# Kernel tuning notes

Measured on AMD Instinct MI355X. Metric: run time of the kernel, lower is better.

The kernel has to match this reference:

```python
import jax, jax.numpy as jnp
import numpy as np

T = 3          # hparams['T'] message-passing iterations
E = 100000     # num edges (rows of link_state)
M = 200000     # num message pairs
D = 128        # hidden dim of link_state / GRU units
H = 256        # Message MLP hidden width
G = 64         # num graphs


def setup_inputs() -> dict:
    key = jax.random.key(0)
    ks = jax.random.split(key, 16)
    s = 0.05
    inp = {
        'link_state': jax.random.normal(ks[0], (E, D), jnp.float32),
        'states_first': jax.random.randint(ks[1], (M,), 0, E),
        'states_second': jax.random.randint(ks[2], (M,), 0, E),
        'states_graph_ids': jnp.sort(jax.random.randint(ks[3], (E,), 0, G)),
        'sates_num_edges': E,
        # Message MLP: Dense(H, relu) -> Dense(D, relu)
        'mW1': jax.random.normal(ks[4], (2 * D, H), jnp.float32) * s,
        'mb1': jnp.zeros((H,), jnp.float32),
        'mW2': jax.random.normal(ks[5], (H, D), jnp.float32) * s,
        'mb2': jnp.zeros((D,), jnp.float32),
        # GRUCell (keras, reset_after=True): kernel [D,3D], recurrent [D,3D], bias [2,3D]
        'gru_kernel': jax.random.normal(ks[6], (D, 3 * D), jnp.float32) * s,
        'gru_recurrent': jax.random.normal(ks[7], (D, 3 * D), jnp.float32) * s,
        'gru_bias': jnp.zeros((2, 3 * D), jnp.float32),
        # Readout MLP: Dense(H, relu) -> Dense(H, relu) -> Dense(1)
        'rW1': jax.random.normal(ks[8], (D, H), jnp.float32) * s,
        'rb1': jnp.zeros((H,), jnp.float32),
        'rW2': jax.random.normal(ks[9], (H, H), jnp.float32) * s,
        'rb2': jnp.zeros((H,), jnp.float32),
        'rW3': jax.random.normal(ks[10], (H, 1), jnp.float32) * s,
        'rb3': jnp.zeros((1,), jnp.float32),
    }
    return inp


def _gru_step(x, h, kernel, recurrent, bias):
    # keras GRUCell with reset_after=True; gate order: z, r, h
    mx = x @ kernel + bias[0]          # [N, 3D]
    mh = h @ recurrent + bias[1]       # [N, 3D]
    xz, xr, xh = jnp.split(mx, 3, axis=-1)
    hz, hr, hh = jnp.split(mh, 3, axis=-1)
    z = jax.nn.sigmoid(xz + hz)
    r = jax.nn.sigmoid(xr + hr)
    hcand = jnp.tanh(xh + r * hh)
    return z * h + (1.0 - z) * hcand


def reference(link_state, states_first, states_second, states_graph_ids,
              sates_num_edges, mW1, mb1, mW2, mb2,
              gru_kernel, gru_recurrent, gru_bias,
              rW1, rb1, rW2, rb2, rW3, rb3):
    for _ in range(T):
        main_e = link_state[states_first]        # [M, D] gather
        neigh_e = link_state[states_second]      # [M, D] gather
        concat = jnp.concatenate([main_e, neigh_e], axis=1)  # [M, 2D]
        msg = jax.nn.relu(concat @ mW1 + mb1)
        msg = jax.nn.relu(msg @ mW2 + mb2)       # [M, D]
        edges_inputs = jax.ops.segment_sum(msg, states_second,
                                           num_segments=sates_num_edges)  # [E, D]
        link_state = _gru_step(edges_inputs, link_state,
                               gru_kernel, gru_recurrent, gru_bias)
    graph_state = jax.ops.segment_sum(link_state, states_graph_ids,
                                      num_segments=G)  # [G, D]
    r = jax.nn.relu(graph_state @ rW1 + rb1)
    r = jax.nn.relu(r @ rW2 + rb2)
    return r @ rW3 + rb3  # [G, 1]
```

## Files before the change

### kernel.cpp

```cpp
#include <hip/hip_runtime.h>

#define NUM_E 100000
#define NUM_M 200000
#define DIM   128
#define HID   256
#define NG    64
#define TITER 3
#define NB_SCAN 98
#define GS_ER 128
#define TM    64

typedef __attribute__((ext_vector_type(8))) short bf16x8;
typedef __attribute__((ext_vector_type(4))) float f32x4;

__device__ __forceinline__ unsigned short f2bf(float f) {
  unsigned u = __float_as_uint(f);
  u += 0x7FFF + ((u >> 16) & 1);
  return (unsigned short)(u >> 16);
}
__device__ __forceinline__ float bf2f(unsigned short h) {
  return __uint_as_float(((unsigned)h) << 16);
}
__device__ __forceinline__ float sigmoidf_(float v) {
  return 1.f / (1.f + __expf(-v));
}
__device__ __forceinline__ float tanhf_(float u) {
  u = fminf(fmaxf(u, -15.f), 15.f);
  float ex = __expf(-2.f * u);
  return (1.f - ex) / (1.f + ex);
}
__device__ __forceinline__ float relu_(float v) { return fmaxf(v, 0.f); }

__device__ __forceinline__ void acc8(float* xs, bf16x8 v) {
  #pragma unroll
  for (int j = 0; j < 8; ++j) xs[j] += bf2f((unsigned short)v[j]);
}

__device__ __forceinline__ int swzm(int row, int col) {
  return row * 256 + (col ^ ((row & 7) << 3));
}
__device__ __forceinline__ int swzg(int row, int col) {
  return row * 128 + (col ^ ((row & 7) << 3));
}

#define MFMA(a, b, c) __builtin_amdgcn_mfma_f32_16x16x32_bf16((a), (b), (c), 0, 0, 0)

__global__ __launch_bounds__(256) void scan1_kernel(const int* __restrict__ counts,
                                                    int* __restrict__ partials) {
  __shared__ int sh[256];
  int b = blockIdx.x, t = threadIdx.x;
  int i0 = b * 1024 + t * 4;
  int c0 = (i0 + 0 < NUM_E) ? counts[i0 + 0] : 0;
  int c1 = (i0 + 1 < NUM_E) ? counts[i0 + 1] : 0;
  int c2 = (i0 + 2 < NUM_E) ? counts[i0 + 2] : 0;
  int c3 = (i0 + 3 < NUM_E) ? counts[i0 + 3] : 0;
  int tsum = c0 + c1 + c2 + c3;
  sh[t] = tsum;
  __syncthreads();
  for (int off = 1; off < 256; off <<= 1) {
    int v = (t >= off) ? sh[t - off] : 0;
    __syncthreads();
    sh[t] += v;
    __syncthreads();
  }
  if (t == 255) partials[b] = sh[255];
}

__global__ void scan2_kernel(const int* __restrict__ partials, int* __restrict__ base,
                             int* __restrict__ rowptr) {
  if (threadIdx.x == 0) {
    int run = 0;
    for (int b = 0; b < NB_SCAN; ++b) { base[b] = run; run += partials[b]; }
    rowptr[NUM_E] = NUM_M;
  }
}

__global__ __launch_bounds__(256) void scan3_kernel(const int* __restrict__ counts,
                                                    const int* __restrict__ base,
                                                    int* __restrict__ rowptr) {
  __shared__ int sh[256];
  int b = blockIdx.x, t = threadIdx.x;
  int i0 = b * 1024 + t * 4;
  int c0 = (i0 + 0 < NUM_E) ? counts[i0 + 0] : 0;
  int c1 = (i0 + 1 < NUM_E) ? counts[i0 + 1] : 0;
  int c2 = (i0 + 2 < NUM_E) ? counts[i0 + 2] : 0;
  int c3 = (i0 + 3 < NUM_E) ? counts[i0 + 3] : 0;
  int tsum = c0 + c1 + c2 + c3;
  sh[t] = tsum;
  __syncthreads();
  for (int off = 1; off < 256; off <<= 1) {
    int v = (t >= off) ? sh[t - off] : 0;
    __syncthreads();
    sh[t] += v;
    __syncthreads();
  }
  int p = base[b] + (sh[t] - tsum);
  if (i0 + 0 < NUM_E) rowptr[i0 + 0] = p;
  if (i0 + 1 < NUM_E) rowptr[i0 + 1] = p + c0;
  if (i0 + 2 < NUM_E) rowptr[i0 + 2] = p + c0 + c1;
  if (i0 + 3 < NUM_E) rowptr[i0 + 3] = p + c0 + c1 + c2;
}

__global__ void scatter_kernel(const int* __restrict__ second,
                               const int* __restrict__ rowptr,
                               int* __restrict__ cursor, int* __restrict__ order) {
  int m = blockIdx.x * blockDim.x + threadIdx.x;
  if (m < NUM_M) {
    int e = second[m];
    int pos = atomicAdd(&cursor[e], 1);
    int idx = rowptr[e] + pos;
    if (idx < rowptr[e + 1]) order[idx] = m;
  }
}

__device__ __forceinline__ void pack_range(
    const float* __restrict__ srcA, const float* __restrict__ srcB, int KrowsA,
    int N, int src_ld, int col_off, unsigned short* __restrict__ dst, int idx) {
  int l = idx & 63;
  int t = idx >> 6;
  int NF = N / 16;
  int nf = t % NF;
  int ks = t / NF;
  int n = nf * 16 + (l & 15) + col_off;
  int k0 = ks * 32 + (l >> 4) * 8;
  unsigned short o[8];
  #pragma unroll
  for (int j = 0; j < 8; ++j) {
    int k = k0 + j;
    const float* src = (k < KrowsA) ? (srcA + (size_t)k * src_ld)
                                    : (srcB + (size_t)(k - KrowsA) * src_ld);
    o[j] = f2bf(src[n]);
  }
  ushort4* d = (ushort4*)(dst + (size_t)idx * 8);
  d[0] = make_ushort4(o[0], o[1], o[2], o[3]);
  d[1] = make_ushort4(o[4], o[5], o[6], o[7]);
}

__global__ __launch_bounds__(256) void prep_kernel(
    const float4* __restrict__ ls4, ushort4* __restrict__ lsb4, int n4,
    const int* __restrict__ second, int* __restrict__ counts,
    float4* __restrict__ gs4,
    const float* __restrict__ mW1, const float* __restrict__ mW2,
    const float* __restrict__ gk,  const float* __restrict__ gr,
    unsigned short* __restrict__ W1p,  unsigned short* __restrict__ W2p,
    unsigned short* __restrict__ Wzrp, unsigned short* __restrict__ Wkhp,
    unsigned short* __restrict__ Wrhp) {
  int i = blockIdx.x * 256 + threadIdx.x;
  if (i < n4) {
    float4 v = ls4[i];
    ushort4 o;
    o.x = f2bf(v.x); o.y = f2bf(v.y); o.z = f2bf(v.z); o.w = f2bf(v.w);
    lsb4[i] = o;
  }
  if (i < NUM_M) atomicAdd(&counts[second[i]], 1);
  if (i < NG * DIM / 4) gs4[i] = make_float4(0.f, 0.f, 0.f, 0.f);
  if      (i < 8192)  pack_range(mW1, mW1, 256, 256, 256, 0,   W1p,  i);
  else if (i < 12288) pack_range(mW2, mW2, 256, 128, 128, 0,   W2p,  i - 8192);
  else if (i < 20480) pack_range(gk,  gr,  128, 256, 384, 0,   Wzrp, i - 12288);
  else if (i < 22528) pack_range(gk,  gk,  128, 128, 384, 256, Wkhp, i - 20480);
  else if (i < 24576) pack_range(gr,  gr,  128, 128, 384, 256, Wrhp, i - 22528);
}

__global__ __launch_bounds__(512, 2) void msg_kernel(
    const unsigned short* __restrict__ lsb,
    const int* __restrict__ first, const int* __restrict__ second,
    const int* __restrict__ order,
    const unsigned short* __restrict__ W1p,
    const float* __restrict__ b1,
    const unsigned short* __restrict__ W2p,
    const float* __restrict__ b2,
    unsigned short* __restrict__ msgout)
{
  __shared__ unsigned short actL[2][TM * 256];
  __shared__ unsigned short h1s[2][TM * 256];

  const int tid  = threadIdx.x;
  const int wave = tid >> 6;
  const int lane = tid & 63;
  const int c    = lane & 15;
  const int quad = lane >> 4;

  const int sr  = tid >> 5;
  const int shf = (tid >> 4) & 1;
  const int si  = tid & 15;

  const bf16x8* W1f = (const bf16x8*)W1p;
  const bf16x8* W2f = (const bf16x8*)W2p;
  bf16x8 w1r[16];
  #pragma unroll
  for (int ks = 0; ks < 8; ++ks)
    #pragma unroll
    for (int i = 0; i < 2; ++i)
      w1r[ks * 2 + i] = W1f[(ks * 16 + wave * 2 + i) * 64 + lane];
  bf16x8 w2r[8];
  #pragma unroll
  for (int ks = 0; ks < 8; ++ks)
    w2r[ks] = W2f[(ks * 8 + wave) * 64 + lane];

  float4 b1v[2];
  #pragma unroll
  for (int i = 0; i < 2; ++i)
    b1v[i] = *(const float4*)(b1 + (wave * 2 + i) * 16 + quad * 4);
  float4 b2v = *(const float4*)(b2 + wave * 16 + quad * 4);

  const int nTiles = NUM_M / TM;
  const int stride = gridDim.x;
  int tile = blockIdx.x;
  if (tile >= nTiles) return;
  int parity = 0;

  {
    #pragma unroll
    for (int k = 0; k < 4; ++k) {
      int m = order[tile * TM + sr + k * 16];
      int e = shf ? second[m] : first[m];
      bf16x8 v = *(const bf16x8*)(lsb + (size_t)e * DIM + si * 8);
      *(bf16x8*)&actL[0][swzm(sr + k * 16, shf * 128 + si * 8)] = v;
    }
  }
  int en[4] = {0, 0, 0, 0};
  {
    int t1 = tile + stride;
    if (t1 < nTiles) {
      #pragma unroll
      for (int k = 0; k < 4; ++k) {
        int m = order[t1 * TM + sr + k * 16];
        en[k] = shf ? second[m] : first[m];
      }
    }
  }
  __syncthreads();

  while (true) {
    const int m0 = tile * TM;
    const int next  = tile + stride;
    const int next2 = next + stride;
    const bool have_next  = (next < nTiles);
    const bool have_next2 = (next2 < nTiles);

    bf16x8 sv[4];
    if (have_next) {
      #pragma unroll
      for (int k = 0; k < 4; ++k)
        sv[k] = *(const bf16x8*)(lsb + (size_t)en[k] * DIM + si * 8);
    }
    int o[4] = {0, 0, 0, 0};
    if (have_next2) {
      #pragma unroll
      for (int k = 0; k < 4; ++k)
        o[k] = order[next2 * TM + sr + k * 16];
    }

    const unsigned short* ab = &actL[parity][0];
    f32x4 acc[4][2];
    #pragma unroll
    for (int s = 0; s < 4; ++s) { acc[s][0] = (f32x4)(0.f); acc[s][1] = (f32x4)(0.f); }
    #pragma unroll
    for (int ks = 0; ks < 8; ++ks) {
      #pragma unroll
      for (int s = 0; s < 4; ++s) {
        bf16x8 b = *(const bf16x8*)&ab[swzm(s * 16 + c, ks * 32 + quad * 8)];
        acc[s][0] = MFMA(w1r[ks * 2 + 0], b, acc[s][0]);
        acc[s][1] = MFMA(w1r[ks * 2 + 1], b, acc[s][1]);
      }
    }

    if (have_next2) {
      #pragma unroll
      for (int k = 0; k < 4; ++k)
        en[k] = shf ? second[o[k]] : first[o[k]];
    }

    if (have_next) {
      unsigned short* aw = &actL[parity ^ 1][0];
      #pragma unroll
      for (int k = 0; k < 4; ++k)
        *(bf16x8*)&aw[swzm(sr + k * 16, shf * 128 + si * 8)] = sv[k];
    }

    unsigned short* hb = &h1s[parity][0];
    #pragma unroll
    for (int i = 0; i < 2; ++i) {
      int n0 = (wave * 2 + i) * 16 + quad * 4;
      #pragma unroll
      for (int s = 0; s < 4; ++s) {
        ushort4 pk;
        pk.x = f2bf(relu_(acc[s][i][0] + b1v[i].x));
        pk.y = f2bf(relu_(acc[s][i][1] + b1v[i].y));
        pk.z = f2bf(relu_(acc[s][i][2] + b1v[i].z));
        pk.w = f2bf(relu_(acc[s][i][3] + b1v[i].w));
        *(ushort4*)&hb[swzm(s * 16 + c, n0)] = pk;
      }
    }
    __syncthreads();

    f32x4 a2[4];
    #pragma unroll
    for (int s = 0; s < 4; ++s) a2[s] = (f32x4)(0.f);
    #pragma unroll
    for (int ks2 = 0; ks2 < 8; ++ks2) {
      #pragma unroll
      for (int s = 0; s < 4; ++s) {
        bf16x8 b = *(const bf16x8*)&hb[swzm(s * 16 + c, ks2 * 32 + quad * 8)];
        a2[s] = MFMA(w2r[ks2], b, a2[s]);
      }
    }

    {
      int n0 = wave * 16 + quad * 4;
      #pragma unroll
      for (int s = 0; s < 4; ++s) {
        ushort4 pk;
        pk.x = f2bf(relu_(a2[s][0] + b2v.x));
        pk.y = f2bf(relu_(a2[s][1] + b2v.y));
        pk.z = f2bf(relu_(a2[s][2] + b2v.z));
        pk.w = f2bf(relu_(a2[s][3] + b2v.w));
        *(ushort4*)(msgout + (size_t)(m0 + s * 16 + c) * DIM + n0) = pk;
      }
    }

    if (!have_next) break;
    tile = next;
    parity ^= 1;
  }
}

__device__ __forceinline__ ushort4 gru_gate(
    f32x4 az, f32x4 ar, f32x4 axh, f32x4 ahh, ushort4 hraw,
    float4 bz0, float4 br0, float4 bh0, float4 bz1, float4 br1, float4 bh1) {
  float ho[4] = { bf2f(hraw.x), bf2f(hraw.y), bf2f(hraw.z), bf2f(hraw.w) };
  const float* paz  = (const float*)&az;  const float* par  = (const float*)&ar;
  const float* paxh = (const float*)&axh; const float* pahh = (const float*)&ahh;
  const float* pz0 = (const float*)&bz0; const float* pr0 = (const float*)&br0;
  const float* ph0 = (const float*)&bh0; const float* pz1 = (const float*)&bz1;
  const float* pr1 = (const float*)&br1; const float* ph1 = (const float*)&bh1;
  unsigned short o[4];
  #pragma unroll
  for (int j = 0; j < 4; ++j) {
    float z  = sigmoidf_(paz[j] + pz0[j] + pz1[j]);
    float r  = sigmoidf_(par[j] + pr0[j] + pr1[j]);
    float hc = tanhf_(paxh[j] + ph0[j] + r * (pahh[j] + ph1[j]));
    o[j] = f2bf(z * ho[j] + (1.f - z) * hc);
  }
  return make_ushort4(o[0], o[1], o[2], o[3]);
}

__global__ __launch_bounds__(512, 2) void gru_kernel(
    const unsigned short* __restrict__ msgb,
    const int* __restrict__ rowptr,
    unsigned short* __restrict__ lsb,
    const unsigned short* __restrict__ Wzrp,
    const unsigned short* __restrict__ Wkhp,
    const unsigned short* __restrict__ Wrhp,
    const float* __restrict__ gb)
{
  __shared__ unsigned short xfL[2][32 * 128];
  __shared__ unsigned short hfL[2][32 * 128];

  const int tid  = threadIdx.x;
  const int wave = tid >> 6;
  const int lane = tid & 63;
  const int c    = lane & 15;
  const int quad = lane >> 4;

  const bf16x8* Wzrf = (const bf16x8*)Wzrp;
  const bf16x8* Wkhf = (const bf16x8*)Wkhp;
  const bf16x8* Wrhf = (const bf16x8*)Wrhp;
  bf16x8 wz[8], wr[8];
  #pragma unroll
  for (int ks = 0; ks < 8; ++ks) {
    wz[ks] = Wzrf[(ks * 16 + wave) * 64 + lane];
    wr[ks] = Wzrf[(ks * 16 + 8 + wave) * 64 + lane];
  }
  bf16x8 wxh[4], whh[4];
  #pragma unroll
  for (int ks = 0; ks < 4; ++ks) {
    wxh[ks] = Wkhf[(ks * 8 + wave) * 64 + lane];
    whh[ks] = Wrhf[(ks * 8 + wave) * 64 + lane];
  }

  const float4* gbv = (const float4*)gb;
  const int q4 = wave * 4 + quad;
  const float4 b0z = gbv[q4],      b0r = gbv[32 + q4],  b0h = gbv[64 + q4];
  const float4 b1z = gbv[96 + q4], b1r = gbv[128 + q4], b1h = gbv[160 + q4];

  const int el = wave * 4 + (lane >> 4);
  const int li = lane & 15;

  const int nTiles = NUM_E / 32;
  const int stride = gridDim.x;
  int tile = blockIdx.x;
  if (tile >= nTiles) return;
  int par = 0;

  {
    const int e  = tile * 32 + el;
    const int rs = rowptr[e], re = rowptr[e + 1];
    float xs[8];
    #pragma unroll
    for (int j = 0; j < 8; ++j) xs[j] = 0.f;
    bf16x8 hrow = *(const bf16x8*)(lsb + (size_t)e * DIM + li * 8);
    for (int p0 = rs; p0 < re; p0 += 8) {
      const int pm = re - 1;
      bf16x8 tv[8];
      #pragma unroll
      for (int k = 0; k < 8; ++k)
        tv[k] = *(const bf16x8*)(msgb + (size_t)min(p0 + k, pm) * DIM + li * 8);
      #pragma unroll
      for (int k = 0; k < 8; ++k)
        if (p0 + k < re) acc8(xs, tv[k]);
    }
    bf16x8 xv;
    #pragma unroll
    for (int j = 0; j < 8; ++j) xv[j] = (short)f2bf(xs[j]);
    *(bf16x8*)&xfL[0][swzg(el, li * 8)] = xv;
    *(bf16x8*)&hfL[0][swzg(el, li * 8)] = hrow;
  }
  int rs1 = 0, re1 = 0;
  if (tile + stride < nTiles) {
    const int e1 = (tile + stride) * 32 + el;
    rs1 = rowptr[e1]; re1 = rowptr[e1 + 1];
  }
  __syncthreads();

  while (true) {
    const int nextT = tile + stride;
    const bool have_next  = (nextT < nTiles);
    const bool have_next2 = (nextT + stride < nTiles);

    bf16x8 r0, r1, r2, r3, r4, r5, r6, r7, hrow;
    if (have_next) {
      const int e1 = nextT * 32 + el;
      const int pc = min(max(re1 - 1, rs1), NUM_M - 1);
      r0 = *(const bf16x8*)(msgb + (size_t)min(rs1 + 0, pc) * DIM + li * 8);
      r1 = *(const bf16x8*)(msgb + (size_t)min(rs1 + 1, pc) * DIM + li * 8);
      r2 = *(const bf16x8*)(msgb + (size_t)min(rs1 + 2, pc) * DIM + li * 8);
      r3 = *(const bf16x8*)(msgb + (size_t)min(rs1 + 3, pc) * DIM + li * 8);
      r4 = *(const bf16x8*)(msgb + (size_t)min(rs1 + 4, pc) * DIM + li * 8);
      r5 = *(const bf16x8*)(msgb + (size_t)min(rs1 + 5, pc) * DIM + li * 8);
      r6 = *(const bf16x8*)(msgb + (size_t)min(rs1 + 6, pc) * DIM + li * 8);
      r7 = *(const bf16x8*)(msgb + (size_t)min(rs1 + 7, pc) * DIM + li * 8);
      hrow = *(const bf16x8*)(lsb + (size_t)e1 * DIM + li * 8);
    }
    int rs2 = 0, re2 = 0;
    if (have_next2) {
      const int e2 = (nextT + stride) * 32 + el;
      rs2 = rowptr[e2]; re2 = rowptr[e2 + 1];
    }

    const unsigned short* xb = &xfL[par][0];
    const unsigned short* hb = &hfL[par][0];
    f32x4 zA = (f32x4)(0.f), zB = (f32x4)(0.f);
    f32x4 rA = (f32x4)(0.f), rB = (f32x4)(0.f);
    f32x4 xhA = (f32x4)(0.f), xhB = (f32x4)(0.f);
    f32x4 hhA = (f32x4)(0.f), hhB = (f32x4)(0.f);
    #pragma unroll
    for (int ks = 0; ks < 4; ++ks) {
      bf16x8 xA = *(const bf16x8*)&xb[swzg(c,      ks * 32 + quad * 8)];
      bf16x8 xB = *(const bf16x8*)&xb[swzg(16 + c, ks * 32 + quad * 8)];
      bf16x8 hA = *(const bf16x8*)&hb[swzg(c,      ks * 32 + quad * 8)];
      bf16x8 hB = *(const bf16x8*)&hb[swzg(16 + c, ks * 32 + quad * 8)];
      zA  = MFMA(wz[ks],     xA, zA);   zB  = MFMA(wz[ks],     xB, zB);
      rA  = MFMA(wr[ks],     xA, rA);   rB  = MFMA(wr[ks],     xB, rB);
      zA  = MFMA(wz[4 + ks], hA, zA);   zB  = MFMA(wz[4 + ks], hB, zB);
      rA  = MFMA(wr[4 + ks], hA, rA);   rB  = MFMA(wr[4 + ks], hB, rB);
      xhA = MFMA(wxh[ks],    xA, xhA);  xhB = MFMA(wxh[ks],    xB, xhB);
      hhA = MFMA(whh[ks],    hA, hhA);  hhB = MFMA(whh[ks],    hB, hhB);
    }
    {
      const int n0 = wave * 16 + quad * 4;
      ushort4 hrawA = *(const ushort4*)&hb[swzg(c,      n0)];
      ushort4 hrawB = *(const ushort4*)&hb[swzg(16 + c, n0)];
      ushort4 pkA = gru_gate(zA, rA, xhA, hhA, hrawA, b0z, b0r, b0h, b1z, b1r, b1h);
      ushort4 pkB = gru_gate(zB, rB, xhB, hhB, hrawB, b0z, b0r, b0h, b1z, b1r, b1h);
      *(ushort4*)(lsb + (size_t)(tile * 32 + c) * DIM + n0)      = pkA;
      *(ushort4*)(lsb + (size_t)(tile * 32 + 16 + c) * DIM + n0) = pkB;
    }

    if (have_next) {
      float xs[8];
      #pragma unroll
      for (int j = 0; j < 8; ++j) xs[j] = 0.f;
      if (rs1 + 0 < re1) acc8(xs, r0);
      if (rs1 + 1 < re1) acc8(xs, r1);
      if (rs1 + 2 < re1) acc8(xs, r2);
      if (rs1 + 3 < re1) acc8(xs, r3);
      if (rs1 + 4 < re1) acc8(xs, r4);
      if (rs1 + 5 < re1) acc8(xs, r5);
      if (rs1 + 6 < re1) acc8(xs, r6);
      if (rs1 + 7 < re1) acc8(xs, r7);
      for (int p0 = rs1 + 8; p0 < re1; p0 += 8) {
        const int pm = re1 - 1;
        bf16x8 tv[8];
        #pragma unroll
        for (int k = 0; k < 8; ++k)
          tv[k] = *(const bf16x8*)(msgb + (size_t)min(p0 + k, pm) * DIM + li * 8);
        #pragma unroll
        for (int k = 0; k < 8; ++k)
          if (p0 + k < re1) acc8(xs, tv[k]);
      }
      bf16x8 xv;
      #pragma unroll
      for (int j = 0; j < 8; ++j) xv[j] = (short)f2bf(xs[j]);
      *(bf16x8*)&xfL[par ^ 1][swzg(el, li * 8)] = xv;
      *(bf16x8*)&hfL[par ^ 1][swzg(el, li * 8)] = hrow;
    }
    __syncthreads();
    if (!have_next) break;
    tile = nextT;
    par ^= 1;
    rs1 = rs2;
    re1 = re2;
  }
}

__global__ __launch_bounds__(256) void graph_sum_kernel(
    const unsigned short* __restrict__ lsb, const int* __restrict__ gids,
    float* __restrict__ gs) {
  const int t = threadIdx.x;
  const int d = t & 127;
  const int half = t >> 7;
  const int e0 = blockIdx.x * GS_ER;
  const int e1 = min(e0 + GS_ER, NUM_E);
  float acc = 0.f;
  int cur = -1;
  for (int e = e0 + half; e < e1; e += 2) {
    int g = gids[e];
    if (g != cur) {
      if (cur >= 0) atomicAdd(&gs[cur * DIM + d], acc);
      acc = 0.f;
      cur = g;
    }
    acc += bf2f(lsb[(size_t)e * DIM + d]);
  }
  if (cur >= 0) atomicAdd(&gs[cur * DIM + d], acc);
}

__global__ __launch_bounds__(256) void readout_kernel(
    const float* __restrict__ gs,
    const float* __restrict__ rW1, const float* __restrict__ rb1,
    const float* __restrict__ rW2, const float* __restrict__ rb2,
    const float* __restrict__ rW3, const float* __restrict__ rb3,
    float* __restrict__ out) {
  __shared__ float shg[DIM];
  __shared__ float sh1[HID];
  __shared__ float red[HID];
  int g = blockIdx.x, c = threadIdx.x;
  if (c < DIM) shg[c] = gs[g * DIM + c];
  __syncthreads();
  float s = rb1[c];
  for (int k = 0; k < DIM; ++k) s += shg[k] * rW1[k * HID + c];
  sh1[c] = relu_(s);
  __syncthreads();
  s = rb2[c];
  for (int k = 0; k < HID; ++k) s += sh1[k] * rW2[k * HID + c];
  red[c] = relu_(s) * rW3[c];
  __syncthreads();
  for (int off = 128; off > 0; off >>= 1) {
    if (c < off) red[c] += red[c + off];
    __syncthreads();
  }
  if (c == 0) out[g] = red[0] + rb3[0];
}

extern "C" void kernel_launch(void* const* d_in, const int* in_sizes, int n_in,
                              void* d_out, int out_size, void* d_ws, size_t ws_size,
                              hipStream_t stream) {
  float* ls          = (float*)d_in[0];
  const int* first   = (const int*)d_in[1];
  const int* second  = (const int*)d_in[2];
  const int* gids    = (const int*)d_in[3];
  const float* mW1   = (const float*)d_in[5];
  const float* mb1   = (const float*)d_in[6];
  const float* mW2   = (const float*)d_in[7];
  const float* mb2   = (const float*)d_in[8];
  const float* gk    = (const float*)d_in[9];
  const float* gr    = (const float*)d_in[10];
  const float* gb    = (const float*)d_in[11];
  const float* rW1   = (const float*)d_in[12];
  const float* rb1   = (const float*)d_in[13];
  const float* rW2   = (const float*)d_in[14];
  const float* rb2   = (const float*)d_in[15];
  const float* rW3   = (const float*)d_in[16];
  const float* rb3   = (const float*)d_in[17];
  float* out = (float*)d_out;

  char* w = (char*)d_ws;
  unsigned short* msgb = (unsigned short*)w;    w += (size_t)NUM_M * DIM * 2;
  unsigned short* lsb  = (unsigned short*)w;    w += (size_t)NUM_E * DIM * 2;
  float* gs    = (float*)w;                     w += NG * DIM * 4;
  int* counts  = (int*)w;                       w += NUM_E * 4;
  int* cursor  = (int*)w;                       w += NUM_E * 4;
  int* rowptr  = (int*)w;                       w += (NUM_E + 4) * 4;
  int* order   = (int*)w;                       w += NUM_M * 4;
  int* partials= (int*)w;                       w += NB_SCAN * 4;
  int* basep   = (int*)w;                       w += NB_SCAN * 4;
  unsigned short* W1p  = (unsigned short*)w;    w += 256 * 256 * 2;
  unsigned short* W2p  = (unsigned short*)w;    w += 256 * 128 * 2;
  unsigned short* Wzrp = (unsigned short*)w;    w += 256 * 256 * 2;
  unsigned short* Wkhp = (unsigned short*)w;    w += 128 * 128 * 2;
  unsigned short* Wrhp = (unsigned short*)w;    w += 128 * 128 * 2;

  hipMemsetAsync(counts, 0, 2 * (size_t)NUM_E * 4, stream);
  const int n4 = NUM_E * DIM / 4;
  prep_kernel<<<(n4 + 255) / 256, 256, 0, stream>>>(
      (const float4*)ls, (ushort4*)lsb, n4, second, counts, (float4*)gs,
      mW1, mW2, gk, gr, W1p, W2p, Wzrp, Wkhp, Wrhp);

  scan1_kernel<<<NB_SCAN, 256, 0, stream>>>(counts, partials);
  scan2_kernel<<<1, 64, 0, stream>>>(partials, basep, rowptr);
  scan3_kernel<<<NB_SCAN, 256, 0, stream>>>(counts, basep, rowptr);
  scatter_kernel<<<(NUM_M + 255) / 256, 256, 0, stream>>>(second, rowptr, cursor, order);

  for (int t = 0; t < TITER; ++t) {
    msg_kernel<<<256, 512, 0, stream>>>(lsb, first, second, order, W1p, mb1, W2p, mb2, msgb);
    gru_kernel<<<256, 512, 0, stream>>>(msgb, rowptr, lsb, Wzrp, Wkhp, Wrhp, gb);
  }
  graph_sum_kernel<<<(NUM_E + GS_ER - 1) / GS_ER, 256, 0, stream>>>(lsb, gids, gs);
  readout_kernel<<<NG, HID, 0, stream>>>(gs, rW1, rb1, rW2, rb2, rW3, rb3, out);
}
```

Before: 492.7 us.

## Fuse message/GRU iterations and readout into one persistent kernel with grid barriers

Replaces the six per-iteration msg/GRU launches plus the graph-sum and readout launches with one persistent 256-block kernel that separates phases using an atomic-counter grid barrier. Shared memory is reused between phases, and register weight loads are kept inside each phase through an opaque zero offset. This removes launch gaps and tail effects between kernels. In exchange it depends on all 256 blocks being co-resident for the spin barrier, and it loses the restrict qualifiers.

After: 1.029 ms. +108.9%, slower.

```diff
diff --git a/kernel.cpp b/kernel.cpp
--- a/kernel.cpp
+++ b/kernel.cpp
@@ -44,6 +44,17 @@
 }
 
 #define MFMA(a, b, c) __builtin_amdgcn_mfma_f32_16x16x32_bf16((a), (b), (c), 0, 0, 0)
+
+__device__ __forceinline__ void gsync(int* bar, int target) {
+  __threadfence();
+  __syncthreads();
+  if (threadIdx.x == 0) {
+    atomicAdd(bar, 1);
+    while (__hip_atomic_load(bar, __ATOMIC_ACQUIRE, __HIP_MEMORY_SCOPE_AGENT) < target)
+      __builtin_amdgcn_s_sleep(8);
+  }
+  __syncthreads();
+}
 
 __global__ __launch_bounds__(256) void scan1_kernel(const int* __restrict__ counts,
                                                     int* __restrict__ partials) {
@@ -139,13 +150,14 @@
 __global__ __launch_bounds__(256) void prep_kernel(
     const float4* __restrict__ ls4, ushort4* __restrict__ lsb4, int n4,
     const int* __restrict__ second, int* __restrict__ counts,
-    float4* __restrict__ gs4,
+    float4* __restrict__ gs4, int* __restrict__ bar,
     const float* __restrict__ mW1, const float* __restrict__ mW2,
     const float* __restrict__ gk,  const float* __restrict__ gr,
     unsigned short* __restrict__ W1p,  unsigned short* __restrict__ W2p,
     unsigned short* __restrict__ Wzrp, unsigned short* __restrict__ Wkhp,
     unsigned short* __restrict__ Wrhp) {
   int i = blockIdx.x * 256 + threadIdx.x;
+  if (i == 0) *bar = 0;
   if (i < n4) {
     float4 v = ls4[i];
     ushort4 o;
@@ -161,25 +173,19 @@
   else if (i < 24576) pack_range(gr,  gr,  128, 128, 384, 256, Wrhp, i - 22528);
 }
 
-__global__ __launch_bounds__(512, 2) void msg_kernel(
-    const unsigned short* __restrict__ lsb,
-    const int* __restrict__ first, const int* __restrict__ second,
-    const int* __restrict__ order,
-    const unsigned short* __restrict__ W1p,
-    const float* __restrict__ b1,
-    const unsigned short* __restrict__ W2p,
-    const float* __restrict__ b2,
-    unsigned short* __restrict__ msgout)
+__device__ __forceinline__ void msg_phase(
+    unsigned short* act0, unsigned short* act1,
+    unsigned short* h10,  unsigned short* h11,
+    const unsigned short* lsb, const int* first, const int* second,
+    const int* order, const unsigned short* W1p, const float* b1,
+    const unsigned short* W2p, const float* b2, unsigned short* msgout,
+    int zero)
 {
-  __shared__ unsigned short actL[2][TM * 256];
-  __shared__ unsigned short h1s[2][TM * 256];
-
   const int tid  = threadIdx.x;
   const int wave = tid >> 6;
   const int lane = tid & 63;
   const int c    = lane & 15;
   const int quad = lane >> 4;
-
   const int sr  = tid >> 5;
   const int shf = (tid >> 4) & 1;
   const int si  = tid & 15;
@@ -191,17 +197,17 @@
   for (int ks = 0; ks < 8; ++ks)
     #pragma unroll
     for (int i = 0; i < 2; ++i)
-      w1r[ks * 2 + i] = W1f[(ks * 16 + wave * 2 + i) * 64 + lane];
+      w1r[ks * 2 + i] = W1f[(ks * 16 + wave * 2 + i) * 64 + lane + zero];
   bf16x8 w2r[8];
   #pragma unroll
   for (int ks = 0; ks < 8; ++ks)
-    w2r[ks] = W2f[(ks * 8 + wave) * 64 + lane];
+    w2r[ks] = W2f[(ks * 8 + wave) * 64 + lane + zero];
 
   float4 b1v[2];
   #pragma unroll
   for (int i = 0; i < 2; ++i)
-    b1v[i] = *(const float4*)(b1 + (wave * 2 + i) * 16 + quad * 4);
-  float4 b2v = *(const float4*)(b2 + wave * 16 + quad * 4);
+    b1v[i] = *(const float4*)(b1 + (wave * 2 + i) * 16 + quad * 4 + zero);
+  float4 b2v = *(const float4*)(b2 + wave * 16 + quad * 4 + zero);
 
   const int nTiles = NUM_M / TM;
   const int stride = gridDim.x;
@@ -215,7 +221,7 @@
       int m = order[tile * TM + sr + k * 16];
       int e = shf ? second[m] : first[m];
       bf16x8 v = *(const bf16x8*)(lsb + (size_t)e * DIM + si * 8);
-      *(bf16x8*)&actL[0][swzm(sr + k * 16, shf * 128 + si * 8)] = v;
+      *(bf16x8*)&act0[swzm(sr + k * 16, shf * 128 + si * 8)] = v;
     }
   }
   int en[4] = {0, 0, 0, 0};
@@ -251,7 +257,7 @@
         o[k] = order[next2 * TM + sr + k * 16];
     }
 
-    const unsigned short* ab = &actL[parity][0];
+    const unsigned short* ab = parity ? act1 : act0;
     f32x4 acc[4][2];
     #pragma unroll
     for (int s = 0; s < 4; ++s) { acc[s][0] = (f32x4)(0.f); acc[s][1] = (f32x4)(0.f); }
@@ -272,13 +278,13 @@
     }
 
     if (have_next) {
-      unsigned short* aw = &actL[parity ^ 1][0];
+      unsigned short* aw = parity ? act0 : act1;
       #pragma unroll
       for (int k = 0; k < 4; ++k)
         *(bf16x8*)&aw[swzm(sr + k * 16, shf * 128 + si * 8)] = sv[k];
     }
 
-    unsigned short* hb = &h1s[parity][0];
+    unsigned short* hb = parity ? h11 : h10;
     #pragma unroll
     for (int i = 0; i < 2; ++i) {
       int n0 = (wave * 2 + i) * 16 + quad * 4;
@@ -345,18 +351,13 @@
   return make_ushort4(o[0], o[1], o[2], o[3]);
 }
 
-__global__ __launch_bounds__(512, 2) void gru_kernel(
-    const unsigned short* __restrict__ msgb,
-    const int* __restrict__ rowptr,
-    unsigned short* __restrict__ lsb,
-    const unsigned short* __restrict__ Wzrp,
-    const unsigned short* __restrict__ Wkhp,
-    const unsigned short* __restrict__ Wrhp,
-    const float* __restrict__ gb)
+__device__ __forceinline__ void gru_phase(
+    unsigned short* xf0, unsigned short* xf1,
+    unsigned short* hf0, unsigned short* hf1,
+    const unsigned short* msgb, const int* rowptr, unsigned short* lsb,
+    const unsigned short* Wzrp, const unsigned short* Wkhp,
+    const unsigned short* Wrhp, const float* gb, int zero)
 {
-  __shared__ unsigned short xfL[2][32 * 128];
-  __shared__ unsigned short hfL[2][32 * 128];
-
   const int tid  = threadIdx.x;
   const int wave = tid >> 6;
   const int lane = tid & 63;
@@ -369,18 +370,18 @@
   bf16x8 wz[8], wr[8];
   #pragma unroll
   for (int ks = 0; ks < 8; ++ks) {
-    wz[ks] = Wzrf[(ks * 16 + wave) * 64 + lane];
-    wr[ks] = Wzrf[(ks * 16 + 8 + wave) * 64 + lane];
+    wz[ks] = Wzrf[(ks * 16 + wave) * 64 + lane + zero];
+    wr[ks] = Wzrf[(ks * 16 + 8 + wave) * 64 + lane + zero];
   }
   bf16x8 wxh[4], whh[4];
   #pragma unroll
   for (int ks = 0; ks < 4; ++ks) {
-    wxh[ks] = Wkhf[(ks * 8 + wave) * 64 + lane];
-    whh[ks] = Wrhf[(ks * 8 + wave) * 64 + lane];
+    wxh[ks] = Wkhf[(ks * 8 + wave) * 64 + lane + zero];
+    whh[ks] = Wrhf[(ks * 8 + wave) * 64 + lane + zero];
   }
 
   const float4* gbv = (const float4*)gb;
-  const int q4 = wave * 4 + quad;
+  const int q4 = wave * 4 + quad + zero;
   const float4 b0z = gbv[q4],      b0r = gbv[32 + q4],  b0h = gbv[64 + q4];
   const float4 b1z = gbv[96 + q4], b1r = gbv[128 + q4], b1h = gbv[160 + q4];
 
@@ -413,8 +414,8 @@
     bf16x8 xv;
     #pragma unroll
     for (int j = 0; j < 8; ++j) xv[j] = (short)f2bf(xs[j]);
-    *(bf16x8*)&xfL[0][swzg(el, li * 8)] = xv;
-    *(bf16x8*)&hfL[0][swzg(el, li * 8)] = hrow;
+    *(bf16x8*)&xf0[swzg(el, li * 8)] = xv;
+    *(bf16x8*)&hf0[swzg(el, li * 8)] = hrow;
   }
   int rs1 = 0, re1 = 0;
   if (tile + stride < nTiles) {
@@ -448,8 +449,8 @@
       rs2 = rowptr[e2]; re2 = rowptr[e2 + 1];
     }
 
-    const unsigned short* xb = &xfL[par][0];
-    const unsigned short* hb = &hfL[par][0];
+    const unsigned short* xb = par ? xf1 : xf0;
+    const unsigned short* hb = par ? hf1 : hf0;
     f32x4 zA = (f32x4)(0.f), zB = (f32x4)(0.f);
     f32x4 rA = (f32x4)(0.f), rB = (f32x4)(0.f);
     f32x4 xhA = (f32x4)(0.f), xhB = (f32x4)(0.f);
@@ -502,8 +503,10 @@
       bf16x8 xv;
       #pragma unroll
       for (int j = 0; j < 8; ++j) xv[j] = (short)f2bf(xs[j]);
-      *(bf16x8*)&xfL[par ^ 1][swzg(el, li * 8)] = xv;
-      *(bf16x8*)&hfL[par ^ 1][swzg(el, li * 8)] = hrow;
+      unsigned short* xw = par ? xf0 : xf1;
+      unsigned short* hw = par ? hf0 : hf1;
+      *(bf16x8*)&xw[swzg(el, li * 8)] = xv;
+      *(bf16x8*)&hw[swzg(el, li * 8)] = hrow;
     }
     __syncthreads();
     if (!have_next) break;
@@ -514,53 +517,80 @@
   }
 }
 
-__global__ __launch_bounds__(256) void graph_sum_kernel(
-    const unsigned short* __restrict__ lsb, const int* __restrict__ gids,
-    float* __restrict__ gs) {
-  const int t = threadIdx.x;
-  const int d = t & 127;
-  const int half = t >> 7;
-  const int e0 = blockIdx.x * GS_ER;
-  const int e1 = min(e0 + GS_ER, NUM_E);
-  float acc = 0.f;
-  int cur = -1;
-  for (int e = e0 + half; e < e1; e += 2) {
-    int g = gids[e];
-    if (g != cur) {
+__global__ __launch_bounds__(512, 2) void loop_kernel(
+    unsigned short* lsb, const int* first, const int* second, const int* order,
+    const unsigned short* W1p, const float* mb1,
+    const unsigned short* W2p, const float* mb2,
+    unsigned short* msgb, const int* rowptr,
+    const unsigned short* Wzrp, const unsigned short* Wkhp,
+    const unsigned short* Wrhp, const float* gb,
+    const int* gids, float* gs,
+    const float* rW1, const float* rb1, const float* rW2, const float* rb2,
+    const float* rW3, const float* rb3, float* out, int* bar)
+{
+  __shared__ unsigned short smA[2][TM * 256];
+  __shared__ unsigned short smB[2][TM * 256];
+
+  int phase = 0;
+  for (int it = 0; it < TITER; ++it) {
+    int z1 = 0; asm volatile("" : "+v"(z1));
+    msg_phase(&smA[0][0], &smA[1][0], &smB[0][0], &smB[1][0],
+              lsb, first, second, order, W1p, mb1, W2p, mb2, msgb, z1);
+    ++phase; gsync(bar, 256 * phase);
+    int z2 = 0; asm volatile("" : "+v"(z2));
+    gru_phase(&smA[0][0], &smA[0][4096], &smA[1][0], &smA[1][4096],
+              msgb, rowptr, lsb, Wzrp, Wkhp, Wrhp, gb, z2);
+    ++phase; gsync(bar, 256 * phase);
+  }
+
+  {
+    const int t = threadIdx.x;
+    const int d = t & 127;
+    const int q = t >> 7;
+    for (int ch = blockIdx.x; ch < (NUM_E + GS_ER - 1) / GS_ER; ch += gridDim.x) {
+      const int e0 = ch * GS_ER;
+      const int e1 = min(e0 + GS_ER, NUM_E);
+      float acc = 0.f;
+      int cur = -1;
+      for (int e = e0 + q; e < e1; e += 4) {
+        int g = gids[e];
+        if (g != cur) {
+          if (cur >= 0) atomicAdd(&gs[cur * DIM + d], acc);
+          acc = 0.f;
+          cur = g;
+        }
+        acc += bf2f(lsb[(size_t)e * DIM + d]);
+      }
       if (cur >= 0) atomicAdd(&gs[cur * DIM + d], acc);
-      acc = 0.f;
-      cur = g;
-    }
-    acc += bf2f(lsb[(size_t)e * DIM + d]);
-  }
-  if (cur >= 0) atomicAdd(&gs[cur * DIM + d], acc);
-}
-
-__global__ __launch_bounds__(256) void readout_kernel(
-    const float* __restrict__ gs,
-    const float* __restrict__ rW1, const float* __restrict__ rb1,
-    const float* __restrict__ rW2, const float* __restrict__ rb2,
-    const float* __restrict__ rW3, const float* __restrict__ rb3,
-    float* __restrict__ out) {
-  __shared__ float shg[DIM];
-  __shared__ float sh1[HID];
-  __shared__ float red[HID];
-  int g = blockIdx.x, c = threadIdx.x;
-  if (c < DIM) shg[c] = gs[g * DIM + c];
-  __syncthreads();
-  float s = rb1[c];
-  for (int k = 0; k < DIM; ++k) s += shg[k] * rW1[k * HID + c];
-  sh1[c] = relu_(s);
-  __syncthreads();
-  s = rb2[c];
-  for (int k = 0; k < HID; ++k) s += sh1[k] * rW2[k * HID + c];
-  red[c] = relu_(s) * rW3[c];
-  __syncthreads();
-  for (int off = 128; off > 0; off >>= 1) {
-    if (c < off) red[c] += red[c + off];
-    __syncthreads();
-  }
-  if (c == 0) out[g] = red[0] + rb3[0];
+    }
+  }
+  ++phase; gsync(bar, 256 * phase);
+
+  if (blockIdx.x < NG) {
+    float* shg = (float*)&smA[0][0];
+    float* sh1 = shg + DIM;
+    float* red = sh1 + HID;
+    const int g = blockIdx.x, c = threadIdx.x;
+    if (c < DIM) shg[c] = gs[g * DIM + c];
+    __syncthreads();
+    if (c < HID) {
+      float s = rb1[c];
+      for (int k = 0; k < DIM; ++k) s += shg[k] * rW1[k * HID + c];
+      sh1[c] = relu_(s);
+    }
+    __syncthreads();
+    if (c < HID) {
+      float s = rb2[c];
+      for (int k = 0; k < HID; ++k) s += sh1[k] * rW2[k * HID + c];
+      red[c] = relu_(s) * rW3[c];
+    }
+    __syncthreads();
+    for (int off = 128; off > 0; off >>= 1) {
+      if (c < off) red[c] += red[c + off];
+      __syncthreads();
+    }
+    if (c == 0) out[g] = red[0] + rb3[0];
+  }
 }
 
 extern "C" void kernel_launch(void* const* d_in, const int* in_sizes, int n_in,
@@ -595,6 +625,7 @@
   int* order   = (int*)w;                       w += NUM_M * 4;
   int* partials= (int*)w;                       w += NB_SCAN * 4;
   int* basep   = (int*)w;                       w += NB_SCAN * 4;
+  int* bar     = (int*)w;                       w += 16;
   unsigned short* W1p  = (unsigned short*)w;    w += 256 * 256 * 2;
   unsigned short* W2p  = (unsigned short*)w;    w += 256 * 128 * 2;
   unsigned short* Wzrp = (unsigned short*)w;    w += 256 * 256 * 2;
@@ -604,7 +635,7 @@
   hipMemsetAsync(counts, 0, 2 * (size_t)NUM_E * 4, stream);
   const int n4 = NUM_E * DIM / 4;
   prep_kernel<<<(n4 + 255) / 256, 256, 0, stream>>>(
-      (const float4*)ls, (ushort4*)lsb, n4, second, counts, (float4*)gs,
+      (const float4*)ls, (ushort4*)lsb, n4, second, counts, (float4*)gs, bar,
       mW1, mW2, gk, gr, W1p, W2p, Wzrp, Wkhp, Wrhp);
 
   scan1_kernel<<<NB_SCAN, 256, 0, stream>>>(counts, partials);
@@ -612,10 +643,7 @@
   scan3_kernel<<<NB_SCAN, 256, 0, stream>>>(counts, basep, rowptr);
   scatter_kernel<<<(NUM_M + 255) / 256, 256, 0, stream>>>(second, rowptr, cursor, order);
 
-  for (int t = 0; t < TITER; ++t) {
-    msg_kernel<<<256, 512, 0, stream>>>(lsb, first, second, order, W1p, mb1, W2p, mb2, msgb);
-    gru_kernel<<<256, 512, 0, stream>>>(msgb, rowptr, lsb, Wzrp, Wkhp, Wrhp, gb);
-  }
-  graph_sum_kernel<<<(NUM_E + GS_ER - 1) / GS_ER, 256, 0, stream>>>(lsb, gids, gs);
-  readout_kernel<<<NG, HID, 0, stream>>>(gs, rW1, rb1, rW2, rb2, rW3, rb3, out);
-}
+  loop_kernel<<<256, 512, 0, stream>>>(
+      lsb, first, second, order, W1p, mb1, W2p, mb2, msgb, rowptr,
+      Wzrp, Wkhp, Wrhp, gb, gids, gs, rW1, rb1, rW2, rb2, rW3, rb3, out, bar);
+}
```

## Store first/second pairs in CSR order and fuse graph sum into readout

Applied to the files above, without the earlier changes.

The scatter step now writes (first, second) index pairs in sorted order, so the message kernel reads one int2 instead of chasing order→first/second. The graph-level segment sum is folded into the readout kernel: each block binary-searches its graph's range in the sorted ids and reduces rows locally. This removes a launch, the zeroing of the accumulator and the global atomics. The trade-off is that the reduction now runs on only 64 blocks, which limits memory parallelism.

Result: slower. 590.3 us (+19.8%).

```diff
diff --git a/kernel.cpp b/kernel.cpp
--- a/kernel.cpp
+++ b/kernel.cpp
@@ -7,7 +7,6 @@
 #define NG    64
 #define TITER 3
 #define NB_SCAN 98
-#define GS_ER 128
 #define TM    64
 
 typedef __attribute__((ext_vector_type(8))) short bf16x8;
@@ -101,15 +100,16 @@
   if (i0 + 3 < NUM_E) rowptr[i0 + 3] = p + c0 + c1 + c2;
 }
 
-__global__ void scatter_kernel(const int* __restrict__ second,
+__global__ void scatter_kernel(const int* __restrict__ first,
+                               const int* __restrict__ second,
                                const int* __restrict__ rowptr,
-                               int* __restrict__ cursor, int* __restrict__ order) {
+                               int* __restrict__ cursor, int2* __restrict__ fs) {
   int m = blockIdx.x * blockDim.x + threadIdx.x;
   if (m < NUM_M) {
     int e = second[m];
     int pos = atomicAdd(&cursor[e], 1);
     int idx = rowptr[e] + pos;
-    if (idx < rowptr[e + 1]) order[idx] = m;
+    if (idx < rowptr[e + 1]) fs[idx] = make_int2(first[m], e);
   }
 }
 
@@ -139,7 +139,6 @@
 __global__ __launch_bounds__(256) void prep_kernel(
     const float4* __restrict__ ls4, ushort4* __restrict__ lsb4, int n4,
     const int* __restrict__ second, int* __restrict__ counts,
-    float4* __restrict__ gs4,
     const float* __restrict__ mW1, const float* __restrict__ mW2,
     const float* __restrict__ gk,  const float* __restrict__ gr,
     unsigned short* __restrict__ W1p,  unsigned short* __restrict__ W2p,
@@ -153,7 +152,6 @@
     lsb4[i] = o;
   }
   if (i < NUM_M) atomicAdd(&counts[second[i]], 1);
-  if (i < NG * DIM / 4) gs4[i] = make_float4(0.f, 0.f, 0.f, 0.f);
   if      (i < 8192)  pack_range(mW1, mW1, 256, 256, 256, 0,   W1p,  i);
   else if (i < 12288) pack_range(mW2, mW2, 256, 128, 128, 0,   W2p,  i - 8192);
   else if (i < 20480) pack_range(gk,  gr,  128, 256, 384, 0,   Wzrp, i - 12288);
@@ -163,8 +161,7 @@
 
 __global__ __launch_bounds__(512, 2) void msg_kernel(
     const unsigned short* __restrict__ lsb,
-    const int* __restrict__ first, const int* __restrict__ second,
-    const int* __restrict__ order,
+    const int2* __restrict__ fs,
     const unsigned short* __restrict__ W1p,
     const float* __restrict__ b1,
     const unsigned short* __restrict__ W2p,
@@ -212,8 +209,8 @@
   {
     #pragma unroll
     for (int k = 0; k < 4; ++k) {
-      int m = order[tile * TM + sr + k * 16];
-      int e = shf ? second[m] : first[m];
+      int2 p = fs[tile * TM + sr + k * 16];
+      int e = shf ? p.y : p.x;
       bf16x8 v = *(const bf16x8*)(lsb + (size_t)e * DIM + si * 8);
       *(bf16x8*)&actL[0][swzm(sr + k * 16, shf * 128 + si * 8)] = v;
     }
@@ -224,8 +221,8 @@
     if (t1 < nTiles) {
       #pragma unroll
       for (int k = 0; k < 4; ++k) {
-        int m = order[t1 * TM + sr + k * 16];
-        en[k] = shf ? second[m] : first[m];
+        int2 p = fs[t1 * TM + sr + k * 16];
+        en[k] = shf ? p.y : p.x;
       }
     }
   }
@@ -244,11 +241,11 @@
       for (int k = 0; k < 4; ++k)
         sv[k] = *(const bf16x8*)(lsb + (size_t)en[k] * DIM + si * 8);
     }
-    int o[4] = {0, 0, 0, 0};
+    int2 p2[4];
     if (have_next2) {
       #pragma unroll
       for (int k = 0; k < 4; ++k)
-        o[k] = order[next2 * TM + sr + k * 16];
+        p2[k] = fs[next2 * TM + sr + k * 16];
     }
 
     const unsigned short* ab = &actL[parity][0];
@@ -268,7 +265,7 @@
     if (have_next2) {
       #pragma unroll
       for (int k = 0; k < 4; ++k)
-        en[k] = shf ? second[o[k]] : first[o[k]];
+        en[k] = shf ? p2[k].y : p2[k].x;
     }
 
     if (have_next) {
@@ -514,30 +511,8 @@
   }
 }
 
-__global__ __launch_bounds__(256) void graph_sum_kernel(
+__global__ __launch_bounds__(256) void gsum_readout_kernel(
     const unsigned short* __restrict__ lsb, const int* __restrict__ gids,
-    float* __restrict__ gs) {
-  const int t = threadIdx.x;
-  const int d = t & 127;
-  const int half = t >> 7;
-  const int e0 = blockIdx.x * GS_ER;
-  const int e1 = min(e0 + GS_ER, NUM_E);
-  float acc = 0.f;
-  int cur = -1;
-  for (int e = e0 + half; e < e1; e += 2) {
-    int g = gids[e];
-    if (g != cur) {
-      if (cur >= 0) atomicAdd(&gs[cur * DIM + d], acc);
-      acc = 0.f;
-      cur = g;
-    }
-    acc += bf2f(lsb[(size_t)e * DIM + d]);
-  }
-  if (cur >= 0) atomicAdd(&gs[cur * DIM + d], acc);
-}
-
-__global__ __launch_bounds__(256) void readout_kernel(
-    const float* __restrict__ gs,
     const float* __restrict__ rW1, const float* __restrict__ rb1,
     const float* __restrict__ rW2, const float* __restrict__ rb2,
     const float* __restrict__ rW3, const float* __restrict__ rb3,
@@ -545,22 +520,47 @@
   __shared__ float shg[DIM];
   __shared__ float sh1[HID];
   __shared__ float red[HID];
-  int g = blockIdx.x, c = threadIdx.x;
-  if (c < DIM) shg[c] = gs[g * DIM + c];
-  __syncthreads();
-  float s = rb1[c];
-  for (int k = 0; k < DIM; ++k) s += shg[k] * rW1[k * HID + c];
-  sh1[c] = relu_(s);
-  __syncthreads();
-  s = rb2[c];
-  for (int k = 0; k < HID; ++k) s += sh1[k] * rW2[k * HID + c];
-  red[c] = relu_(s) * rW3[c];
+  const int g = blockIdx.x, tid = threadIdx.x;
+  const int d = tid & 127, half = tid >> 7;
+
+  int s0, s1;
+  {
+    int lo = 0, hi = NUM_E;
+    while (lo < hi) { int mid = (lo + hi) >> 1; if (gids[mid] < g) lo = mid + 1; else hi = mid; }
+    s0 = lo;
+    hi = NUM_E;
+    while (lo < hi) { int mid = (lo + hi) >> 1; if (gids[mid] < g + 1) lo = mid + 1; else hi = mid; }
+    s1 = lo;
+  }
+
+  float acc = 0.f;
+  for (int eb = s0 + half; eb < s1; eb += 16) {
+    const int pm = s1 - 1;
+    unsigned short tv[8];
+    #pragma unroll
+    for (int k = 0; k < 8; ++k)
+      tv[k] = lsb[(size_t)min(eb + 2 * k, pm) * DIM + d];
+    #pragma unroll
+    for (int k = 0; k < 8; ++k)
+      if (eb + 2 * k < s1) acc += bf2f(tv[k]);
+  }
+  red[tid] = acc;
+  __syncthreads();
+  if (tid < DIM) shg[tid] = red[tid] + red[tid + DIM];
+  __syncthreads();
+  float s = rb1[tid];
+  for (int k = 0; k < DIM; ++k) s += shg[k] * rW1[k * HID + tid];
+  sh1[tid] = relu_(s);
+  __syncthreads();
+  s = rb2[tid];
+  for (int k = 0; k < HID; ++k) s += sh1[k] * rW2[k * HID + tid];
+  red[tid] = relu_(s) * rW3[tid];
   __syncthreads();
   for (int off = 128; off > 0; off >>= 1) {
-    if (c < off) red[c] += red[c + off];
+    if (tid < off) red[tid] += red[tid + off];
     __syncthreads();
   }
-  if (c == 0) out[g] = red[0] + rb3[0];
+  if (tid == 0) out[g] = red[0] + rb3[0];
 }
 
 extern "C" void kernel_launch(void* const* d_in, const int* in_sizes, int n_in,
@@ -588,11 +588,10 @@
   char* w = (char*)d_ws;
   unsigned short* msgb = (unsigned short*)w;    w += (size_t)NUM_M * DIM * 2;
   unsigned short* lsb  = (unsigned short*)w;    w += (size_t)NUM_E * DIM * 2;
-  float* gs    = (float*)w;                     w += NG * DIM * 4;
   int* counts  = (int*)w;                       w += NUM_E * 4;
   int* cursor  = (int*)w;                       w += NUM_E * 4;
   int* rowptr  = (int*)w;                       w += (NUM_E + 4) * 4;
-  int* order   = (int*)w;                       w += NUM_M * 4;
+  int2* fs     = (int2*)w;                      w += (size_t)NUM_M * 8;
   int* partials= (int*)w;                       w += NB_SCAN * 4;
   int* basep   = (int*)w;                       w += NB_SCAN * 4;
   unsigned short* W1p  = (unsigned short*)w;    w += 256 * 256 * 2;
@@ -604,18 +603,17 @@
   hipMemsetAsync(counts, 0, 2 * (size_t)NUM_E * 4, stream);
   const int n4 = NUM_E * DIM / 4;
   prep_kernel<<<(n4 + 255) / 256, 256, 0, stream>>>(
-      (const float4*)ls, (ushort4*)lsb, n4, second, counts, (float4*)gs,
+      (const float4*)ls, (ushort4*)lsb, n4, second, counts,
       mW1, mW2, gk, gr, W1p, W2p, Wzrp, Wkhp, Wrhp);
 
   scan1_kernel<<<NB_SCAN, 256, 0, stream>>>(counts, partials);
   scan2_kernel<<<1, 64, 0, stream>>>(partials, basep, rowptr);
   scan3_kernel<<<NB_SCAN, 256, 0, stream>>>(counts, basep, rowptr);
-  scatter_kernel<<<(NUM_M + 255) / 256, 256, 0, stream>>>(second, rowptr, cursor, order);
+  scatter_kernel<<<(NUM_M + 255) / 256, 256, 0, stream>>>(first, second, rowptr, cursor, fs);
 
   for (int t = 0; t < TITER; ++t) {
-    msg_kernel<<<256, 512, 0, stream>>>(lsb, first, second, order, W1p, mb1, W2p, mb2, msgb);
+    msg_kernel<<<256, 512, 0, stream>>>(lsb, fs, W1p, mb1, W2p, mb2, msgb);
     gru_kernel<<<256, 512, 0, stream>>>(msgb, rowptr, lsb, Wzrp, Wkhp, Wrhp, gb);
   }
-  graph_sum_kernel<<<(NUM_E + GS_ER - 1) / GS_ER, 256, 0, stream>>>(lsb, gids, gs);
-  readout_kernel<<<NG, HID, 0, stream>>>(gs, rW1, rb1, rW2, rb2, rW3, rb3, out);
-}
+  gsum_readout_kernel<<<NG, HID, 0, stream>>>(lsb, gids, rW1, rb1, rW2, rb2, rW3, rb3, out);
+}
```
